# Kernel optimization log

Measured on AMD Instinct MI355X. Metric: run time of the kernel, lower is better.

Reference implementation:

```python
import jax, jax.numpy as jnp
import numpy as np

N_NODES = 20000
N_EDGES = 100000
N_SNAP = 2
N_DIM, E_DIM, OUT_DIM, HEADS = 64, 32, 64, 2


def edge_gat(x, ef, src, dst, Wn, We, al, ar, ae, b):
    # DGL EdgeGATConv: fc (no bias), edge-aware attention, edge softmax over
    # incoming edges, message = (ft_src + ft_edge) * alpha, final additive bias.
    H, D = al.shape
    ft = (x @ Wn).reshape(-1, H, D)                # [N,H,D]
    fe = (ef @ We).reshape(-1, H, D)               # [E,H,D]
    el = jnp.einsum('nhd,hd->nh', ft, al)          # [N,H]
    er = jnp.einsum('nhd,hd->nh', ft, ar)          # [N,H]
    ee = jnp.einsum('ehd,hd->eh', fe, ae)          # [E,H]
    logits = jax.nn.leaky_relu(el[src] + er[dst] + ee, 0.2)  # [E,H]
    m = jax.ops.segment_max(logits, dst, num_segments=N_NODES)
    p = jnp.exp(logits - m[dst])
    s = jax.ops.segment_sum(p, dst, num_segments=N_NODES)
    a = p / s[dst]                                 # edge softmax per dst node
    msg = (ft[src] + fe) * a[..., None]            # [E,H,D]
    return jax.ops.segment_sum(msg, dst, num_segments=N_NODES) + b  # [N,H,D]


def gnn_rnn(x, ef, src, dst, params):
    # GNN_RNN.forward per snapshot: stacked EdgeGAT layers, head-mean each.
    for (Wn, We, al, ar, ae, b) in params:
        x = edge_gat(x, ef, src, dst, Wn, We, al, ar, ae, b).mean(axis=1)
    return x


def _mk_layer(key, in_d, e_d, out_d, heads, scale=0.1):
    ks = jax.random.split(key, 6)
    return dict(
        Wn=jax.random.normal(ks[0], (in_d, heads * out_d), jnp.float32) * scale,
        We=jax.random.normal(ks[1], (e_d, heads * out_d), jnp.float32) * scale,
        al=jax.random.normal(ks[2], (heads, out_d), jnp.float32) * scale,
        ar=jax.random.normal(ks[3], (heads, out_d), jnp.float32) * scale,
        ae=jax.random.normal(ks[4], (heads, out_d), jnp.float32) * scale,
        b=jax.random.normal(ks[5], (heads, out_d), jnp.float32) * scale,
    )


def setup_inputs() -> dict:
    key = jax.random.key(0)
    ks = jax.random.split(key, 10)
    inp = {
        'x': jax.random.normal(ks[0], (N_SNAP, N_NODES, N_DIM), jnp.float32),
        'e': jax.random.normal(ks[1], (N_SNAP, N_EDGES, E_DIM), jnp.float32),
        'src': jax.random.randint(ks[2], (N_SNAP, N_EDGES), 0, N_NODES),
        'dst': jax.random.randint(ks[3], (N_SNAP, N_EDGES), 0, N_NODES),
    }
    enc0 = _mk_layer(ks[4], N_DIM, E_DIM, OUT_DIM, HEADS)
    enc1 = _mk_layer(ks[5], OUT_DIM, E_DIM, OUT_DIM, HEADS)
    dec0 = _mk_layer(ks[6], OUT_DIM, E_DIM, N_DIM, HEADS)
    dec1 = _mk_layer(ks[7], N_DIM, E_DIM, N_DIM, HEADS)
    for pref, lp in [('enc0', enc0), ('enc1', enc1), ('dec0', dec0), ('dec1', dec1)]:
        for k, v in lp.items():
            inp[f'{pref}_{k}'] = v
    inp['W_e2d'] = jax.random.normal(ks[8], (OUT_DIM, OUT_DIM), jnp.float32) * 0.1
    return inp


def reference(x, e, src, dst,
              enc0_Wn, enc0_We, enc0_al, enc0_ar, enc0_ae, enc0_b,
              enc1_Wn, enc1_We, enc1_al, enc1_ar, enc1_ae, enc1_b,
              W_e2d,
              dec0_Wn, dec0_We, dec0_al, dec0_ar, dec0_ae, dec0_b,
              dec1_Wn, dec1_We, dec1_al, dec1_ar, dec1_ae, dec1_b):
    enc_params = [(enc0_Wn, enc0_We, enc0_al, enc0_ar, enc0_ae, enc0_b),
                  (enc1_Wn, enc1_We, enc1_al, enc1_ar, enc1_ae, enc1_b)]
    dec_params = [(dec0_Wn, dec0_We, dec0_al, dec0_ar, dec0_ae, dec0_b),
                  (dec1_Wn, dec1_We, dec1_al, dec1_ar, dec1_ae, dec1_b)]

    def per_snapshot(xs, es, ss, ds):
        h = gnn_rnn(xs, es, ss, ds, enc_params)   # encoder, [N,out_dim]
        h = h @ W_e2d.T                           # encoder_to_decoder (no bias)
        return gnn_rnn(h, es, ss, ds, dec_params) # decoder, [N,n_dim]

    decoded = jax.vmap(per_snapshot)(x, e, src, dst)  # [S,N,n_dim]
    return decoded[-1]
```

## Files before the change

kernel.cpp:

```cpp
#include <hip/hip_runtime.h>
#include <math.h>

#define N_NODES 20000
#define N_EDGES 100000

__device__ __forceinline__ float rl_f(float v, int l) {
    return __uint_as_float(__builtin_amdgcn_readlane(__float_as_uint(v), l));
}
__device__ __forceinline__ int rl_i(int v, int l) {
    return __builtin_amdgcn_readlane(v, l);
}
__device__ __forceinline__ float lrelu(float x) { return x > 0.f ? x : 0.2f * x; }

__global__ __launch_bounds__(256) void count_kernel(const int* __restrict__ dst,
                                                    int* __restrict__ cnt,
                                                    int* __restrict__ pos) {
    int e = blockIdx.x * 256 + threadIdx.x;
    if (e < N_EDGES) pos[e] = atomicAdd(&cnt[dst[e]], 1);
}

__global__ __launch_bounds__(256) void scanA_kernel(const int* __restrict__ cnt,
                                                    int* __restrict__ bsum) {
    __shared__ int wsum[4];
    const int tid = threadIdx.x;
    int idx = blockIdx.x * 256 + tid;
    int v = (idx < N_NODES) ? cnt[idx] : 0;
    int s = v;
#pragma unroll
    for (int off = 32; off; off >>= 1) s += __shfl_xor(s, off);
    if ((tid & 63) == 0) wsum[tid >> 6] = s;
    __syncthreads();
    if (tid == 0) bsum[blockIdx.x] = wsum[0] + wsum[1] + wsum[2] + wsum[3];
}

__global__ __launch_bounds__(256) void scanC_kernel(const int* __restrict__ cnt,
                                                    const int* __restrict__ bsum,
                                                    int* __restrict__ row_ptr) {
    __shared__ int sdata[256];
    __shared__ int s_boff;
    const int tid = threadIdx.x;
    const int b = blockIdx.x;
    int idx = b * 256 + tid;
    int v = (idx < N_NODES) ? cnt[idx] : 0;
    sdata[tid] = v;
    if (tid < 64) {
        int a = (tid < b) ? bsum[tid] : 0;
        if (64 + tid < b) a += bsum[64 + tid];
#pragma unroll
        for (int off = 32; off; off >>= 1) a += __shfl_xor(a, off);
        if (tid == 0) s_boff = a;
    }
    __syncthreads();
    for (int off = 1; off < 256; off <<= 1) {
        int t_ = (tid >= off) ? sdata[tid - off] : 0;
        __syncthreads();
        sdata[tid] += t_;
        __syncthreads();
    }
    if (idx < N_NODES) row_ptr[idx] = s_boff + sdata[tid] - v;
    if (b == 0 && tid == 0) row_ptr[N_NODES] = N_EDGES;
}

__global__ __launch_bounds__(256) void params_kernel(
    const float* __restrict__ Wn0, const float* __restrict__ al0, const float* __restrict__ ar0,
    const float* __restrict__ Wn1, const float* __restrict__ al1, const float* __restrict__ ar1,
    const float* __restrict__ dWn, const float* __restrict__ al2, const float* __restrict__ ar2,
    const float* __restrict__ Wn3, const float* __restrict__ al3, const float* __restrict__ ar3,
    const float* __restrict__ W_e2d,
    const float* __restrict__ We0, const float* __restrict__ ae0,
    const float* __restrict__ We1, const float* __restrict__ ae1,
    const float* __restrict__ We2, const float* __restrict__ ae2,
    const float* __restrict__ We3, const float* __restrict__ ae3,
    const float* __restrict__ X0,
    float* __restrict__ P4, float* __restrict__ Wcomb, float* __restrict__ Q,
    float2* __restrict__ EL2, float2* __restrict__ ER2) {
    __shared__ float praw[256];
    const int b = blockIdx.x;
    const int t = threadIdx.x;

    if (b < 4) {
        const int L = b;
        if (L != 2) {
            const float* Wn = (L == 0) ? Wn0 : (L == 1) ? Wn1 : Wn3;
            const float* al = (L == 0) ? al0 : (L == 1) ? al1 : al3;
            const float* ar = (L == 0) ? ar0 : (L == 1) ? ar1 : ar3;
            const int k = t >> 2, o = t & 3;
            const float* a = (o & 2) ? ar : al;
            const int h = o & 1;
            float acc = 0.f;
#pragma unroll 8
            for (int d = 0; d < 64; d++) acc = fmaf(Wn[k * 128 + h * 64 + d], a[h * 64 + d], acc);
            P4[L * 256 + t] = acc;
        } else {
            {
                const int i = t >> 2, o = t & 3;
                const float* a = (o & 2) ? ar2 : al2;
                const int h = o & 1;
                float acc = 0.f;
#pragma unroll 8
                for (int d = 0; d < 64; d++) acc = fmaf(dWn[i * 128 + h * 64 + d], a[h * 64 + d], acc);
                praw[t] = acc;
            }
            __syncthreads();
            const int j = t >> 2, o = t & 3;
            float acc = 0.f;
#pragma unroll 8
            for (int i = 0; i < 64; i++) acc = fmaf(W_e2d[i * 64 + j], praw[i * 4 + o], acc);
            P4[2 * 256 + t] = acc;
        }
    } else if (b < 36) {
        int idx = (b - 4) * 256 + t;
        int j = idx >> 7, c = idx & 127;
        float acc = 0.f;
#pragma unroll 8
        for (int i = 0; i < 64; i++) acc = fmaf(W_e2d[i * 64 + j], dWn[i * 128 + c], acc);
        Wcomb[idx] = acc;
    } else if (b == 36) {
        const int k = t >> 3, o = t & 7, L = o >> 1, h = o & 1;
        const float* We = (L == 0) ? We0 : (L == 1) ? We1 : (L == 2) ? We2 : We3;
        const float* ae = (L == 0) ? ae0 : (L == 1) ? ae1 : (L == 2) ? ae2 : ae3;
        float acc = 0.f;
#pragma unroll 8
        for (int d = 0; d < 64; d++) acc = fmaf(We[k * 128 + h * 64 + d], ae[h * 64 + d], acc);
        Q[t] = acc;
    } else {
        {
            const int k = t >> 2, o = t & 3;
            const float* a = (o & 2) ? ar0 : al0;
            const int h = o & 1;
            float acc = 0.f;
#pragma unroll 8
            for (int d = 0; d < 64; d++) acc = fmaf(Wn0[k * 128 + h * 64 + d], a[h * 64 + d], acc);
            praw[t] = acc;
        }
        __syncthreads();
        const int lane = t & 63;
        const int wave = t >> 6;
        const float px = praw[lane * 4 + 0], py = praw[lane * 4 + 1];
        const float pz = praw[lane * 4 + 2], pw = praw[lane * 4 + 3];
        const int nb = gridDim.x - 37;
        for (int node = (b - 37) * 4 + wave; node < N_NODES; node += nb * 4) {
            float xv = X0[node * 64 + lane];
            float e0 = xv * px, e1 = xv * py, f0 = xv * pz, f1 = xv * pw;
#pragma unroll
            for (int off = 32; off; off >>= 1) {
                e0 += __shfl_xor(e0, off);
                e1 += __shfl_xor(e1, off);
                f0 += __shfl_xor(f0, off);
                f1 += __shfl_xor(f1, off);
            }
            if (lane == 0) {
                EL2[node] = make_float2(e0, e1);
                ER2[node] = make_float2(f0, f1);
            }
        }
    }
}

__global__ __launch_bounds__(256) void prep_kernel(const float* __restrict__ Efeat,
                                                   const int* __restrict__ src,
                                                   const int* __restrict__ dst,
                                                   const int* __restrict__ pos,
                                                   const int* __restrict__ row_ptr,
                                                   const float* __restrict__ Q,
                                                   float* __restrict__ E_csr,
                                                   int* __restrict__ src_csr,
                                                   float* __restrict__ EE_csr) {
    __shared__ float QS[256];
    __shared__ float ES[32][33];
    __shared__ int JS[32];
    const int tid = threadIdx.x;
    QS[tid] = Q[tid];
    const int e0 = blockIdx.x * 32;
    const int el_ = tid >> 3, quad = tid & 7;
    float4 v = ((const float4*)Efeat)[(size_t)(e0 + el_) * 8 + quad];
    ES[el_][quad * 4 + 0] = v.x;
    ES[el_][quad * 4 + 1] = v.y;
    ES[el_][quad * 4 + 2] = v.z;
    ES[el_][quad * 4 + 3] = v.w;
    if (tid < 32) {
        int e = e0 + tid;
        int j = row_ptr[dst[e]] + pos[e];
        JS[tid] = j;
        src_csr[j] = src[e];
    }
    __syncthreads();
    const int j = JS[el_];
    ((float4*)E_csr)[(size_t)j * 8 + quad] = v;
    const int o = quad;
    float acc = 0.f;
#pragma unroll
    for (int k = 0; k < 32; k++) acc = fmaf(ES[el_][k], QS[k * 8 + o], acc);
    EE_csr[(size_t)(o >> 1) * 2 * N_EDGES + (size_t)j * 2 + (o & 1)] = acc;
}

__global__ __launch_bounds__(256) void gather_kernel(const float* __restrict__ X,
                                                     const float2* __restrict__ EL2,
                                                     const float2* __restrict__ ER2,
                                                     const float* __restrict__ E_csr,
                                                     const int* __restrict__ src_csr,
                                                     const int* __restrict__ row_ptr,
                                                     const float2* __restrict__ EE_L,
                                                     float2* __restrict__ AX2,
                                                     float* __restrict__ AE) {
    const int tid = threadIdx.x;
    const int lane = tid & 63;
    const int node = blockIdx.x * 4 + (tid >> 6);
    if (node >= N_NODES) return;
    const int half = lane >> 5, hl = lane & 31;

    const int beg = row_ptr[node], end = row_ptr[node + 1];
    const int deg = end - beg;
    if (deg == 0) {
        AX2[node * 64 + lane] = make_float2(0.f, 0.f);
        AE[node * 64 + lane] = 0.f;
        return;
    }
    const float2 er = ER2[node];
    float l0 = 0.f, l1 = 0.f, aX0 = 0.f, aX1 = 0.f, aE = 0.f;

    if (deg <= 64) {
        int sn = 0;
        float w0 = 0.f, w1 = 0.f;
        if (lane < deg) {
            sn = src_csr[beg + lane];
            float2 ee = EE_L[beg + lane];
            float2 el = EL2[sn];
            w0 = __expf(lrelu(el.x + er.x + ee.x));
            w1 = __expf(lrelu(el.y + er.y + ee.y));
        }
        l0 = w0;
        l1 = w1;
#pragma unroll
        for (int off = 32; off; off >>= 1) {
            l0 += __shfl_xor(l0, off);
            l1 += __shfl_xor(l1, off);
        }
        const int dm1 = deg - 1;
        {
            float xs[8], es[8];
#pragma unroll
            for (int t = 0; t < 8; t++) {
                int ct = t < dm1 ? t : dm1;
                int st = rl_i(sn, ct);
                xs[t] = X[st * 64 + lane];
                es[t] = E_csr[(size_t)(beg + ct) * 32 + hl];
            }
#pragma unroll
            for (int t = 0; t < 8; t++) {
                float w0t = rl_f(w0, t);
                float w1t = rl_f(w1, t);
                aX0 = fmaf(w0t, xs[t], aX0);
                aX1 = fmaf(w1t, xs[t], aX1);
                aE = fmaf(half ? w1t : w0t, es[t], aE);
            }
        }
        int t = 8;
        for (; t + 4 <= deg; t += 4) {
            int s0 = rl_i(sn, t), s1 = rl_i(sn, t + 1);
            int s2 = rl_i(sn, t + 2), s3 = rl_i(sn, t + 3);
            float x0 = X[s0 * 64 + lane];
            float x1 = X[s1 * 64 + lane];
            float x2 = X[s2 * 64 + lane];
            float x3 = X[s3 * 64 + lane];
            const float* Eb = E_csr + (size_t)(beg + t) * 32 + hl;
            float e0 = Eb[0], e1 = Eb[32], e2 = Eb[64], e3 = Eb[96];
            float w00 = rl_f(w0, t), w01 = rl_f(w0, t + 1);
            float w02 = rl_f(w0, t + 2), w03 = rl_f(w0, t + 3);
            float w10 = rl_f(w1, t), w11 = rl_f(w1, t + 1);
            float w12 = rl_f(w1, t + 2), w13 = rl_f(w1, t + 3);
            aX0 = fmaf(w00, x0, aX0); aX1 = fmaf(w10, x0, aX1);
            aX0 = fmaf(w01, x1, aX0); aX1 = fmaf(w11, x1, aX1);
            aX0 = fmaf(w02, x2, aX0); aX1 = fmaf(w12, x2, aX1);
            aX0 = fmaf(w03, x3, aX0); aX1 = fmaf(w13, x3, aX1);
            aE = fmaf(half ? w10 : w00, e0, aE);
            aE = fmaf(half ? w11 : w01, e1, aE);
            aE = fmaf(half ? w12 : w02, e2, aE);
            aE = fmaf(half ? w13 : w03, e3, aE);
        }
        for (; t < deg; t++) {
            int st = rl_i(sn, t);
            float w0t = rl_f(w0, t), w1t = rl_f(w1, t);
            float xv = X[st * 64 + lane];
            float ev = E_csr[(size_t)(beg + t) * 32 + hl];
            aX0 = fmaf(w0t, xv, aX0);
            aX1 = fmaf(w1t, xv, aX1);
            aE = fmaf(half ? w1t : w0t, ev, aE);
        }
    } else {
        for (int c = beg; c < end; c += 64) {
            int j = c + lane;
            int sn_ = 0;
            float w0c = 0.f, w1c = 0.f;
            if (j < end) {
                sn_ = src_csr[j];
                float2 ee = EE_L[j];
                float2 el = EL2[sn_];
                w0c = __expf(lrelu(el.x + er.x + ee.x));
                w1c = __expf(lrelu(el.y + er.y + ee.y));
            }
            float s0 = w0c, s1 = w1c;
#pragma unroll
            for (int off = 32; off; off >>= 1) {
                s0 += __shfl_xor(s0, off);
                s1 += __shfl_xor(s1, off);
            }
            l0 += s0;
            l1 += s1;
            int nch = (end - c) < 64 ? (end - c) : 64;
            int t = 0;
            for (; t + 4 <= nch; t += 4) {
                int q0 = rl_i(sn_, t), q1 = rl_i(sn_, t + 1);
                int q2 = rl_i(sn_, t + 2), q3 = rl_i(sn_, t + 3);
                float x0 = X[q0 * 64 + lane];
                float x1 = X[q1 * 64 + lane];
                float x2 = X[q2 * 64 + lane];
                float x3 = X[q3 * 64 + lane];
                const float* Eb = E_csr + (size_t)(c + t) * 32 + hl;
                float e0 = Eb[0], e1 = Eb[32], e2 = Eb[64], e3 = Eb[96];
                float w00 = rl_f(w0c, t), w01 = rl_f(w0c, t + 1);
                float w02 = rl_f(w0c, t + 2), w03 = rl_f(w0c, t + 3);
                float w10 = rl_f(w1c, t), w11 = rl_f(w1c, t + 1);
                float w12 = rl_f(w1c, t + 2), w13 = rl_f(w1c, t + 3);
                aX0 = fmaf(w00, x0, aX0); aX1 = fmaf(w10, x0, aX1);
                aX0 = fmaf(w01, x1, aX0); aX1 = fmaf(w11, x1, aX1);
                aX0 = fmaf(w02, x2, aX0); aX1 = fmaf(w12, x2, aX1);
                aX0 = fmaf(w03, x3, aX0); aX1 = fmaf(w13, x3, aX1);
                aE = fmaf(half ? w10 : w00, e0, aE);
                aE = fmaf(half ? w11 : w01, e1, aE);
                aE = fmaf(half ? w12 : w02, e2, aE);
                aE = fmaf(half ? w13 : w03, e3, aE);
            }
            for (; t < nch; t++) {
                int st = rl_i(sn_, t);
                float w0t = rl_f(w0c, t), w1t = rl_f(w1c, t);
                float xv = X[st * 64 + lane];
                float ev = E_csr[(size_t)(c + t) * 32 + hl];
                aX0 = fmaf(w0t, xv, aX0);
                aX1 = fmaf(w1t, xv, aX1);
                aE = fmaf(half ? w1t : w0t, ev, aE);
            }
        }
    }
    const float inv0 = l0 > 0.f ? 1.f / l0 : 0.f;
    const float inv1 = l1 > 0.f ? 1.f / l1 : 0.f;
    AX2[node * 64 + lane] = make_float2(aX0 * inv0, aX1 * inv1);
    AE[node * 64 + lane] = aE * (half ? inv1 : inv0);
}

__global__ __launch_bounds__(256) void epilogue_kernel(const float2* __restrict__ AX2,
                                                       const float* __restrict__ AE,
                                                       const float* __restrict__ Wn,
                                                       const float* __restrict__ We,
                                                       const float* __restrict__ bias,
                                                       const float* __restrict__ P4next,
                                                       const int has_next,
                                                       float* __restrict__ OUT,
                                                       float2* __restrict__ EL2,
                                                       float2* __restrict__ ER2) {
    __shared__ float4 WnS4[32 * 64];
    __shared__ float4 WeS4[16 * 64];
    const int tid = threadIdx.x;
    for (int idx = tid; idx < 32 * 64; idx += 256) {
        int k2 = idx >> 6, l = idx & 63;
        WnS4[idx] = make_float4(Wn[(2 * k2) * 128 + l], Wn[(2 * k2) * 128 + 64 + l],
                                Wn[(2 * k2 + 1) * 128 + l], Wn[(2 * k2 + 1) * 128 + 64 + l]);
    }
    for (int idx = tid; idx < 16 * 64; idx += 256) {
        int k2 = idx >> 6, l = idx & 63;
        WeS4[idx] = make_float4(We[(2 * k2) * 128 + l], We[(2 * k2) * 128 + 64 + l],
                                We[(2 * k2 + 1) * 128 + l], We[(2 * k2 + 1) * 128 + 64 + l]);
    }
    __syncthreads();
    const int lane = tid & 63;
    const int wave = tid >> 6;
    const float b0 = bias[lane], b1 = bias[64 + lane];
    const float4 p = has_next ? ((const float4*)P4next)[lane] : make_float4(0.f, 0.f, 0.f, 0.f);

    for (int base = blockIdx.x * 8 + wave * 2; base < N_NODES; base += gridDim.x * 8) {
        const int n0 = base, n1 = base + 1;
        float2 axa = AX2[n0 * 64 + lane];
        float2 axb = AX2[n1 * 64 + lane];
        float aea = AE[n0 * 64 + lane];
        float aeb = AE[n1 * 64 + lane];
        float r0a = 0.f, r1a = 0.f, r0b = 0.f, r1b = 0.f;
#pragma unroll
        for (int k2 = 0; k2 < 32; k2++) {
            float4 w4 = WnS4[k2 * 64 + lane];
            float a00 = rl_f(axa.x, 2 * k2), a01 = rl_f(axa.x, 2 * k2 + 1);
            float a10 = rl_f(axa.y, 2 * k2), a11 = rl_f(axa.y, 2 * k2 + 1);
            float c00 = rl_f(axb.x, 2 * k2), c01 = rl_f(axb.x, 2 * k2 + 1);
            float c10 = rl_f(axb.y, 2 * k2), c11 = rl_f(axb.y, 2 * k2 + 1);
            r0a = fmaf(a00, w4.x, r0a); r1a = fmaf(a10, w4.y, r1a);
            r0a = fmaf(a01, w4.z, r0a); r1a = fmaf(a11, w4.w, r1a);
            r0b = fmaf(c00, w4.x, r0b); r1b = fmaf(c10, w4.y, r1b);
            r0b = fmaf(c01, w4.z, r0b); r1b = fmaf(c11, w4.w, r1b);
        }
#pragma unroll
        for (int k2 = 0; k2 < 16; k2++) {
            float4 w4 = WeS4[k2 * 64 + lane];
            float a00 = rl_f(aea, 2 * k2), a01 = rl_f(aea, 2 * k2 + 1);
            float a10 = rl_f(aea, 32 + 2 * k2), a11 = rl_f(aea, 32 + 2 * k2 + 1);
            float c00 = rl_f(aeb, 2 * k2), c01 = rl_f(aeb, 2 * k2 + 1);
            float c10 = rl_f(aeb, 32 + 2 * k2), c11 = rl_f(aeb, 32 + 2 * k2 + 1);
            r0a = fmaf(a00, w4.x, r0a); r1a = fmaf(a10, w4.y, r1a);
            r0a = fmaf(a01, w4.z, r0a); r1a = fmaf(a11, w4.w, r1a);
            r0b = fmaf(c00, w4.x, r0b); r1b = fmaf(c10, w4.y, r1b);
            r0b = fmaf(c01, w4.z, r0b); r1b = fmaf(c11, w4.w, r1b);
        }
        float outa = 0.5f * (r0a + b0 + r1a + b1);
        float outb = 0.5f * (r0b + b0 + r1b + b1);
        OUT[n0 * 64 + lane] = outa;
        OUT[n1 * 64 + lane] = outb;
        if (has_next) {
            float e0a = outa * p.x, e1a = outa * p.y, f0a = outa * p.z, f1a = outa * p.w;
            float e0b = outb * p.x, e1b = outb * p.y, f0b = outb * p.z, f1b = outb * p.w;
#pragma unroll
            for (int off = 32; off; off >>= 1) {
                e0a += __shfl_xor(e0a, off); e1a += __shfl_xor(e1a, off);
                f0a += __shfl_xor(f0a, off); f1a += __shfl_xor(f1a, off);
                e0b += __shfl_xor(e0b, off); e1b += __shfl_xor(e1b, off);
                f0b += __shfl_xor(f0b, off); f1b += __shfl_xor(f1b, off);
            }
            if (lane == 0) {
                EL2[n0] = make_float2(e0a, e1a);
                ER2[n0] = make_float2(f0a, f1a);
                EL2[n1] = make_float2(e0b, e1b);
                ER2[n1] = make_float2(f0b, f1b);
            }
        }
    }
}

extern "C" void kernel_launch(void* const* d_in, const int* in_sizes, int n_in,
                              void* d_out, int out_size, void* d_ws, size_t ws_size,
                              hipStream_t stream) {
    const float* x = (const float*)d_in[0];
    const float* e = (const float*)d_in[1];
    const int* src = (const int*)d_in[2];
    const int* dst = (const int*)d_in[3];

    const float* x1 = x + (size_t)1 * N_NODES * 64;
    const float* e1 = e + (size_t)1 * N_EDGES * 32;
    const int* src1 = src + N_EDGES;
    const int* dst1 = dst + N_EDGES;

    int we2d_idx, dec0_b, dec1_b;
    if (in_sizes[16] == 64 * 64 && in_sizes[17] == 64 * 128) {
        we2d_idx = 16; dec0_b = 17; dec1_b = 23;
    } else {
        dec0_b = 16; dec1_b = 22; we2d_idx = 28;
    }
    auto P = [&](int i) { return (const float*)d_in[i]; };

    char* ws = (char*)d_ws;
    int* cnt      = (int*)(ws + 0);
    int* row_ptr  = (int*)(ws + 80000);
    int* pos      = (int*)(ws + 160064);
    int* bsum     = (int*)(ws + 560064);
    float* q      = (float*)(ws + 560576);
    int* src_csr  = (int*)(ws + 561600);
    float* e_csr  = (float*)(ws + 961600);
    float* ee_csr = (float*)(ws + 13761600);
    float* p4_all = (float*)(ws + 16961600);
    float* el     = (float*)(ws + 16965696);
    float* er     = (float*)(ws + 17125696);
    float* ax     = (float*)(ws + 17285696);
    float* ae     = (float*)(ws + 27525696);
    float* h      = (float*)(ws + 32645696);
    float* wcomb  = (float*)(ws + 37765696);

    hipMemsetAsync(cnt, 0, N_NODES * sizeof(int), stream);
    const int EB = (N_EDGES + 255) / 256;
    const int SB = (N_NODES + 255) / 256;
    count_kernel<<<EB, 256, 0, stream>>>(dst1, cnt, pos);
    scanA_kernel<<<SB, 256, 0, stream>>>(cnt, bsum);
    scanC_kernel<<<SB, 256, 0, stream>>>(cnt, bsum, row_ptr);

    params_kernel<<<512, 256, 0, stream>>>(
        P(4), P(6), P(7),
        P(10), P(12), P(13),
        P(dec0_b + 0), P(dec0_b + 2), P(dec0_b + 3),
        P(dec1_b + 0), P(dec1_b + 2), P(dec1_b + 3),
        P(we2d_idx),
        P(5), P(8), P(11), P(14),
        P(dec0_b + 1), P(dec0_b + 4), P(dec1_b + 1), P(dec1_b + 4),
        x1,
        p4_all, wcomb, q, (float2*)el, (float2*)er);

    prep_kernel<<<N_EDGES / 32, 256, 0, stream>>>(e1, src1, dst1, pos, row_ptr, q,
                                                  e_csr, src_csr, ee_csr);

    const int NB_G = (N_NODES + 3) / 4;
    const int NB_E = 768;

    auto run_layer = [&](const float* Xin, const float* Wn, const float* We_,
                         const float* b_, int L, float* Out) {
        gather_kernel<<<NB_G, 256, 0, stream>>>(
            Xin, (const float2*)el, (const float2*)er, e_csr, src_csr, row_ptr,
            (const float2*)(ee_csr) + (size_t)L * N_EDGES, (float2*)ax, ae);
        epilogue_kernel<<<NB_E, 256, 0, stream>>>(
            (const float2*)ax, ae, Wn, We_, b_, p4_all + (L + 1) * 256, (L < 3) ? 1 : 0,
            Out, (float2*)el, (float2*)er);
    };

    run_layer(x1, P(4), P(5), P(9), 0, h);
    run_layer(h, P(10), P(11), P(15), 1, h);
    run_layer(h, wcomb, P(dec0_b + 1), P(dec0_b + 5), 2, h);
    run_layer(h, P(dec1_b + 0), P(dec1_b + 1), P(dec1_b + 5), 3, (float*)d_out);
}
```

Baseline: 315.3 us.

## Fold count reset into params kernel, single-pass scan, 4-node epilogue

Removes the memset by zeroing the count array and the scan state flags inside params_kernel. The two-kernel scan is merged into one kernel that uses a decoupled lookback over per-block flagged sums. The epilogue now processes four nodes per wave instead of two to reuse each shared-memory weight load, with the grid set to 625 blocks so 16-node strides divide evenly. The aim is fewer launches and more work per weight load, at the cost of spin-waiting in the scan and higher register pressure in the epilogue.

```diff
diff --git a/kernel.cpp b/kernel.cpp
--- a/kernel.cpp
+++ b/kernel.cpp
@@ -11,55 +11,6 @@
     return __builtin_amdgcn_readlane(v, l);
 }
 __device__ __forceinline__ float lrelu(float x) { return x > 0.f ? x : 0.2f * x; }
-
-__global__ __launch_bounds__(256) void count_kernel(const int* __restrict__ dst,
-                                                    int* __restrict__ cnt,
-                                                    int* __restrict__ pos) {
-    int e = blockIdx.x * 256 + threadIdx.x;
-    if (e < N_EDGES) pos[e] = atomicAdd(&cnt[dst[e]], 1);
-}
-
-__global__ __launch_bounds__(256) void scanA_kernel(const int* __restrict__ cnt,
-                                                    int* __restrict__ bsum) {
-    __shared__ int wsum[4];
-    const int tid = threadIdx.x;
-    int idx = blockIdx.x * 256 + tid;
-    int v = (idx < N_NODES) ? cnt[idx] : 0;
-    int s = v;
-#pragma unroll
-    for (int off = 32; off; off >>= 1) s += __shfl_xor(s, off);
-    if ((tid & 63) == 0) wsum[tid >> 6] = s;
-    __syncthreads();
-    if (tid == 0) bsum[blockIdx.x] = wsum[0] + wsum[1] + wsum[2] + wsum[3];
-}
-
-__global__ __launch_bounds__(256) void scanC_kernel(const int* __restrict__ cnt,
-                                                    const int* __restrict__ bsum,
-                                                    int* __restrict__ row_ptr) {
-    __shared__ int sdata[256];
-    __shared__ int s_boff;
-    const int tid = threadIdx.x;
-    const int b = blockIdx.x;
-    int idx = b * 256 + tid;
-    int v = (idx < N_NODES) ? cnt[idx] : 0;
-    sdata[tid] = v;
-    if (tid < 64) {
-        int a = (tid < b) ? bsum[tid] : 0;
-        if (64 + tid < b) a += bsum[64 + tid];
-#pragma unroll
-        for (int off = 32; off; off >>= 1) a += __shfl_xor(a, off);
-        if (tid == 0) s_boff = a;
-    }
-    __syncthreads();
-    for (int off = 1; off < 256; off <<= 1) {
-        int t_ = (tid >= off) ? sdata[tid - off] : 0;
-        __syncthreads();
-        sdata[tid] += t_;
-        __syncthreads();
-    }
-    if (idx < N_NODES) row_ptr[idx] = s_boff + sdata[tid] - v;
-    if (b == 0 && tid == 0) row_ptr[N_NODES] = N_EDGES;
-}
 
 __global__ __launch_bounds__(256) void params_kernel(
     const float* __restrict__ Wn0, const float* __restrict__ al0, const float* __restrict__ ar0,
@@ -73,7 +24,8 @@
     const float* __restrict__ We3, const float* __restrict__ ae3,
     const float* __restrict__ X0,
     float* __restrict__ P4, float* __restrict__ Wcomb, float* __restrict__ Q,
-    float2* __restrict__ EL2, float2* __restrict__ ER2) {
+    float2* __restrict__ EL2, float2* __restrict__ ER2,
+    int* __restrict__ cnt, unsigned* __restrict__ state) {
     __shared__ float praw[256];
     const int b = blockIdx.x;
     const int t = threadIdx.x;
@@ -124,6 +76,9 @@
         for (int d = 0; d < 64; d++) acc = fmaf(We[k * 128 + h * 64 + d], ae[h * 64 + d], acc);
         Q[t] = acc;
     } else {
+        const int nb = gridDim.x - 37;
+        for (int i = (b - 37) * 256 + t; i < N_NODES; i += nb * 256) cnt[i] = 0;
+        if (b == 37 && t < 128) state[t] = 0u;
         {
             const int k = t >> 2, o = t & 3;
             const float* a = (o & 2) ? ar0 : al0;
@@ -138,7 +93,6 @@
         const int wave = t >> 6;
         const float px = praw[lane * 4 + 0], py = praw[lane * 4 + 1];
         const float pz = praw[lane * 4 + 2], pw = praw[lane * 4 + 3];
-        const int nb = gridDim.x - 37;
         for (int node = (b - 37) * 4 + wave; node < N_NODES; node += nb * 4) {
             float xv = X0[node * 64 + lane];
             float e0 = xv * px, e1 = xv * py, f0 = xv * pz, f1 = xv * pw;
@@ -155,6 +109,55 @@
             }
         }
     }
+}
+
+__global__ __launch_bounds__(256) void count_kernel(const int* __restrict__ dst,
+                                                    int* __restrict__ cnt,
+                                                    int* __restrict__ pos) {
+    int e = blockIdx.x * 256 + threadIdx.x;
+    if (e < N_EDGES) pos[e] = atomicAdd(&cnt[dst[e]], 1);
+}
+
+__global__ __launch_bounds__(256) void scan_kernel(const int* __restrict__ cnt,
+                                                   unsigned* __restrict__ state,
+                                                   int* __restrict__ row_ptr) {
+    __shared__ int sdata[256];
+    __shared__ int s_boff;
+    const int tid = threadIdx.x;
+    const int b = blockIdx.x;
+    int idx = b * 256 + tid;
+    int v = (idx < N_NODES) ? cnt[idx] : 0;
+    sdata[tid] = v;
+    __syncthreads();
+    for (int off = 1; off < 256; off <<= 1) {
+        int t_ = (tid >= off) ? sdata[tid - off] : 0;
+        __syncthreads();
+        sdata[tid] += t_;
+        __syncthreads();
+    }
+    if (tid == 0)
+        __hip_atomic_store(&state[b], (unsigned)sdata[255] | 0x80000000u,
+                           __ATOMIC_RELEASE, __HIP_MEMORY_SCOPE_AGENT);
+    if (tid < 64) {
+        unsigned a = 0, c = 0;
+        if (tid < b) {
+            do {
+                a = __hip_atomic_load(&state[tid], __ATOMIC_ACQUIRE, __HIP_MEMORY_SCOPE_AGENT);
+            } while (!(a & 0x80000000u));
+        }
+        if (64 + tid < b) {
+            do {
+                c = __hip_atomic_load(&state[64 + tid], __ATOMIC_ACQUIRE, __HIP_MEMORY_SCOPE_AGENT);
+            } while (!(c & 0x80000000u));
+        }
+        int s = (int)(a & 0x3FFFFFFFu) + (int)(c & 0x3FFFFFFFu);
+#pragma unroll
+        for (int off = 32; off; off >>= 1) s += __shfl_xor(s, off);
+        if (tid == 0) s_boff = s;
+    }
+    __syncthreads();
+    if (idx < N_NODES) row_ptr[idx] = s_boff + sdata[tid] - v;
+    if (b == 0 && tid == 0) row_ptr[N_NODES] = N_EDGES;
 }
 
 __global__ __launch_bounds__(256) void prep_kernel(const float* __restrict__ Efeat,
@@ -377,56 +380,64 @@
     const float b0 = bias[lane], b1 = bias[64 + lane];
     const float4 p = has_next ? ((const float4*)P4next)[lane] : make_float4(0.f, 0.f, 0.f, 0.f);
 
-    for (int base = blockIdx.x * 8 + wave * 2; base < N_NODES; base += gridDim.x * 8) {
-        const int n0 = base, n1 = base + 1;
-        float2 axa = AX2[n0 * 64 + lane];
-        float2 axb = AX2[n1 * 64 + lane];
-        float aea = AE[n0 * 64 + lane];
-        float aeb = AE[n1 * 64 + lane];
-        float r0a = 0.f, r1a = 0.f, r0b = 0.f, r1b = 0.f;
+    for (int base = blockIdx.x * 16 + wave * 4; base < N_NODES; base += gridDim.x * 16) {
+        float2 ax[4];
+        float ae4[4];
+#pragma unroll
+        for (int j = 0; j < 4; j++) {
+            ax[j] = AX2[(base + j) * 64 + lane];
+            ae4[j] = AE[(base + j) * 64 + lane];
+        }
+        float r0[4] = {0.f, 0.f, 0.f, 0.f};
+        float r1[4] = {0.f, 0.f, 0.f, 0.f};
 #pragma unroll
         for (int k2 = 0; k2 < 32; k2++) {
             float4 w4 = WnS4[k2 * 64 + lane];
-            float a00 = rl_f(axa.x, 2 * k2), a01 = rl_f(axa.x, 2 * k2 + 1);
-            float a10 = rl_f(axa.y, 2 * k2), a11 = rl_f(axa.y, 2 * k2 + 1);
-            float c00 = rl_f(axb.x, 2 * k2), c01 = rl_f(axb.x, 2 * k2 + 1);
-            float c10 = rl_f(axb.y, 2 * k2), c11 = rl_f(axb.y, 2 * k2 + 1);
-            r0a = fmaf(a00, w4.x, r0a); r1a = fmaf(a10, w4.y, r1a);
-            r0a = fmaf(a01, w4.z, r0a); r1a = fmaf(a11, w4.w, r1a);
-            r0b = fmaf(c00, w4.x, r0b); r1b = fmaf(c10, w4.y, r1b);
-            r0b = fmaf(c01, w4.z, r0b); r1b = fmaf(c11, w4.w, r1b);
+#pragma unroll
+            for (int j = 0; j < 4; j++) {
+                float a00 = rl_f(ax[j].x, 2 * k2), a01 = rl_f(ax[j].x, 2 * k2 + 1);
+                float a10 = rl_f(ax[j].y, 2 * k2), a11 = rl_f(ax[j].y, 2 * k2 + 1);
+                r0[j] = fmaf(a00, w4.x, r0[j]);
+                r1[j] = fmaf(a10, w4.y, r1[j]);
+                r0[j] = fmaf(a01, w4.z, r0[j]);
+                r1[j] = fmaf(a11, w4.w, r1[j]);
+            }
         }
 #pragma unroll
         for (int k2 = 0; k2 < 16; k2++) {
             float4 w4 = WeS4[k2 * 64 + lane];
-            float a00 = rl_f(aea, 2 * k2), a01 = rl_f(aea, 2 * k2 + 1);
-            float a10 = rl_f(aea, 32 + 2 * k2), a11 = rl_f(aea, 32 + 2 * k2 + 1);
-            float c00 = rl_f(aeb, 2 * k2), c01 = rl_f(aeb, 2 * k2 + 1);
-            float c10 = rl_f(aeb, 32 + 2 * k2), c11 = rl_f(aeb, 32 + 2 * k2 + 1);
-            r0a = fmaf(a00, w4.x, r0a); r1a = fmaf(a10, w4.y, r1a);
-            r0a = fmaf(a01, w4.z, r0a); r1a = fmaf(a11, w4.w, r1a);
-            r0b = fmaf(c00, w4.x, r0b); r1b = fmaf(c10, w4.y, r1b);
-            r0b = fmaf(c01, w4.z, r0b); r1b = fmaf(c11, w4.w, r1b);
-        }
-        float outa = 0.5f * (r0a + b0 + r1a + b1);
-        float outb = 0.5f * (r0b + b0 + r1b + b1);
-        OUT[n0 * 64 + lane] = outa;
-        OUT[n1 * 64 + lane] = outb;
+#pragma unroll
+            for (int j = 0; j < 4; j++) {
+                float a00 = rl_f(ae4[j], 2 * k2), a01 = rl_f(ae4[j], 2 * k2 + 1);
+                float a10 = rl_f(ae4[j], 32 + 2 * k2), a11 = rl_f(ae4[j], 32 + 2 * k2 + 1);
+                r0[j] = fmaf(a00, w4.x, r0[j]);
+                r1[j] = fmaf(a10, w4.y, r1[j]);
+                r0[j] = fmaf(a01, w4.z, r0[j]);
+                r1[j] = fmaf(a11, w4.w, r1[j]);
+            }
+        }
+        float outv[4];
+#pragma unroll
+        for (int j = 0; j < 4; j++) {
+            outv[j] = 0.5f * (r0[j] + b0 + r1[j] + b1);
+            OUT[(base + j) * 64 + lane] = outv[j];
+        }
         if (has_next) {
-            float e0a = outa * p.x, e1a = outa * p.y, f0a = outa * p.z, f1a = outa * p.w;
-            float e0b = outb * p.x, e1b = outb * p.y, f0b = outb * p.z, f1b = outb * p.w;
-#pragma unroll
-            for (int off = 32; off; off >>= 1) {
-                e0a += __shfl_xor(e0a, off); e1a += __shfl_xor(e1a, off);
-                f0a += __shfl_xor(f0a, off); f1a += __shfl_xor(f1a, off);
-                e0b += __shfl_xor(e0b, off); e1b += __shfl_xor(e1b, off);
-                f0b += __shfl_xor(f0b, off); f1b += __shfl_xor(f1b, off);
-            }
-            if (lane == 0) {
-                EL2[n0] = make_float2(e0a, e1a);
-                ER2[n0] = make_float2(f0a, f1a);
-                EL2[n1] = make_float2(e0b, e1b);
-                ER2[n1] = make_float2(f0b, f1b);
+#pragma unroll
+            for (int j = 0; j < 4; j++) {
+                float e0 = outv[j] * p.x, e1 = outv[j] * p.y;
+                float f0 = outv[j] * p.z, f1 = outv[j] * p.w;
+#pragma unroll
+                for (int off = 32; off; off >>= 1) {
+                    e0 += __shfl_xor(e0, off);
+                    e1 += __shfl_xor(e1, off);
+                    f0 += __shfl_xor(f0, off);
+                    f1 += __shfl_xor(f1, off);
+                }
+                if (lane == 0) {
+                    EL2[base + j] = make_float2(e0, e1);
+                    ER2[base + j] = make_float2(f0, f1);
+                }
             }
         }
     }
@@ -454,28 +465,21 @@
     auto P = [&](int i) { return (const float*)d_in[i]; };
 
     char* ws = (char*)d_ws;
-    int* cnt      = (int*)(ws + 0);
-    int* row_ptr  = (int*)(ws + 80000);
-    int* pos      = (int*)(ws + 160064);
-    int* bsum     = (int*)(ws + 560064);
-    float* q      = (float*)(ws + 560576);
-    int* src_csr  = (int*)(ws + 561600);
-    float* e_csr  = (float*)(ws + 961600);
-    float* ee_csr = (float*)(ws + 13761600);
-    float* p4_all = (float*)(ws + 16961600);
-    float* el     = (float*)(ws + 16965696);
-    float* er     = (float*)(ws + 17125696);
-    float* ax     = (float*)(ws + 17285696);
-    float* ae     = (float*)(ws + 27525696);
-    float* h      = (float*)(ws + 32645696);
-    float* wcomb  = (float*)(ws + 37765696);
-
-    hipMemsetAsync(cnt, 0, N_NODES * sizeof(int), stream);
-    const int EB = (N_EDGES + 255) / 256;
-    const int SB = (N_NODES + 255) / 256;
-    count_kernel<<<EB, 256, 0, stream>>>(dst1, cnt, pos);
-    scanA_kernel<<<SB, 256, 0, stream>>>(cnt, bsum);
-    scanC_kernel<<<SB, 256, 0, stream>>>(cnt, bsum, row_ptr);
+    int* cnt        = (int*)(ws + 0);
+    int* row_ptr    = (int*)(ws + 80000);
+    int* pos        = (int*)(ws + 160064);
+    unsigned* state = (unsigned*)(ws + 560064);
+    float* q        = (float*)(ws + 560576);
+    int* src_csr    = (int*)(ws + 561600);
+    float* e_csr    = (float*)(ws + 961600);
+    float* ee_csr   = (float*)(ws + 13761600);
+    float* p4_all   = (float*)(ws + 16961600);
+    float* el       = (float*)(ws + 16965696);
+    float* er       = (float*)(ws + 17125696);
+    float* ax       = (float*)(ws + 17285696);
+    float* ae       = (float*)(ws + 27525696);
+    float* h        = (float*)(ws + 32645696);
+    float* wcomb    = (float*)(ws + 37765696);
 
     params_kernel<<<512, 256, 0, stream>>>(
         P(4), P(6), P(7),
@@ -486,13 +490,17 @@
         P(5), P(8), P(11), P(14),
         P(dec0_b + 1), P(dec0_b + 4), P(dec1_b + 1), P(dec1_b + 4),
         x1,
-        p4_all, wcomb, q, (float2*)el, (float2*)er);
-
+        p4_all, wcomb, q, (float2*)el, (float2*)er, cnt, state);
+
+    const int EB = (N_EDGES + 255) / 256;
+    const int SB = (N_NODES + 255) / 256;
+    count_kernel<<<EB, 256, 0, stream>>>(dst1, cnt, pos);
+    scan_kernel<<<SB, 256, 0, stream>>>(cnt, state, row_ptr);
     prep_kernel<<<N_EDGES / 32, 256, 0, stream>>>(e1, src1, dst1, pos, row_ptr, q,
                                                   e_csr, src_csr, ee_csr);
 
     const int NB_G = (N_NODES + 3) / 4;
-    const int NB_E = 768;
+    const int NB_E = 625;
 
     auto run_layer = [&](const float* Xin, const float* Wn, const float* We_,
                          const float* b_, int L, float* Out) {
```

After: 320.8 us. No clear change (+1.8%).
